# Kernel tuning notes

Hardware: AMD Instinct MI355X
Metric: run time of the kernel (lower is better)

Reference implementation:

```python
import jax, jax.numpy as jnp
import numpy as np

B, C, H, W = 32, 256, 64, 64
LN_EPS = 1e-5

def _conv1x1(x, w, b=None):
    # x: (b,c,h,w), w: (out,c) -> (b,out,h,w)
    y = jnp.einsum('bchw,oc->bohw', x, w)
    if b is not None:
        y = y + b[None, :, None, None]
    return y

def _hsigmoid(t):
    # mmcv HSigmoid: clamp((x + 3) / 6, 0, 1)
    return jnp.clip((t + 3.0) / 6.0, 0.0, 1.0)

def setup_inputs() -> dict:
    key = jax.random.key(0)
    ks = jax.random.split(key, 12)
    s = 0.05
    return {
        'x': jax.random.normal(ks[0], (B, C, H, W), jnp.float32),
        'conv0_w': jax.random.normal(ks[1], (C // 2, C), jnp.float32) * s,
        'conv0_b': jnp.zeros((C // 2,), jnp.float32),
        'bn1_w': jax.random.normal(ks[2], (C, C // 2), jnp.float32) * s,
        'bn1_b': jnp.zeros((C,), jnp.float32),
        'conv1_w': jax.random.normal(ks[3], (1, C), jnp.float32) * s,
        'conv1_b': jnp.zeros((1,), jnp.float32),
        'ln_g': jnp.ones((C,), jnp.float32),
        'ln_b': jnp.zeros((C,), jnp.float32),
        'sk_w1': jax.random.normal(ks[4], (C // 2, C), jnp.float32) * s,
        'sk_w2': jax.random.normal(ks[5], (C, C // 2), jnp.float32) * s,
        'res_w': jax.random.normal(ks[6], (C, C), jnp.float32) * s,
        'res_b': jnp.zeros((C,), jnp.float32),
    }

def reference(x, conv0_w, conv0_b, bn1_w, bn1_b, conv1_w, conv1_b,
              ln_g, ln_b, sk_w1, sk_w2, res_w, res_b):
    b, c, h, w = x.shape
    # ---- channel attention ----
    ca = _conv1x1(x, conv0_w, conv0_b)               # (b, c/2, h, w)
    ca = ca.mean(axis=(2, 3), keepdims=True)          # GAP -> (b, c/2, 1, 1)
    ca = _conv1x1(ca, bn1_w, bn1_b)                   # (b, c, 1, 1)
    ca = _hsigmoid(ca)
    v = ca.reshape(b, c)                              # nchw_to_nlc -> (b, 1, c); LN over c
    mu = v.mean(axis=-1, keepdims=True)
    var = ((v - mu) ** 2).mean(axis=-1, keepdims=True)
    v = (v - mu) * jax.lax.rsqrt(var + LN_EPS) * ln_g + ln_b
    ca = v.reshape(b, c, 1, 1)
    # ---- spatial attention ----
    sa = _conv1x1(x, conv1_w, conv1_b)                # (b, 1, h, w)
    # ---- parallel attention ----
    par = _hsigmoid(sa + ca)                          # (b, c, h, w)
    # ---- sequence attention: bmm outer product (b,c,1)x(b,1,hw) ----
    seq = _hsigmoid(ca * sa)                          # (b, c, h, w)
    # ---- SK module ----
    u = (seq + par).mean(axis=(2, 3), keepdims=True)  # GAP -> (b, c, 1, 1)
    u = _conv1x1(u, sk_w1)                            # (b, c/2, 1, 1), no bias
    u = _conv1x1(u, sk_w2)                            # (b, c, 1, 1), no bias
    a = jax.nn.softmax(u, axis=1)
    sk = seq * a + par * (1.0 - a)
    # softmax over spatial (nchw_to_nlc + Softmax(dim=1))
    sk = jax.nn.softmax(sk.reshape(b, c, h * w), axis=2).reshape(b, c, h, w)
    selected = x * sk
    # ---- self attention ----
    self_attn = selected.sum(axis=(2, 3)).reshape(b, c, 1, 1) + _conv1x1(x, res_w, res_b)
    return selected + self_attn
```

## Files before the change

kernel.cpp:

```cpp
#include <hip/hip_runtime.h>
#include <math.h>

#define B_  32
#define C_  256
#define HW_ 4096
#define LN_EPS 1e-5f

typedef __attribute__((ext_vector_type(4))) float f32x4;
typedef __attribute__((ext_vector_type(8))) short bf16x8;
typedef __attribute__((ext_vector_type(4))) unsigned u32x4;

__device__ __forceinline__ float hsig(float v) {
    return fminf(fmaxf((v + 3.0f) * (1.0f / 6.0f), 0.0f), 1.0f);
}
__device__ __forceinline__ float tval(float ca, float a, float sav) {
    return a * hsig(ca * sav) + (1.0f - a) * hsig(ca + sav);
}
__device__ __forceinline__ unsigned short f2bf(float f) {
    unsigned u = __float_as_uint(f);
    unsigned r = (u + 0x7fffu + ((u >> 16) & 1u)) >> 16;
    return (unsigned short)r;
}
__device__ __forceinline__ float bf2f(unsigned short h) {
    return __uint_as_float(((unsigned)h) << 16);
}


__global__ __launch_bounds__(256) void k_pass1t(
    const float* __restrict__ x, const float* __restrict__ w1,
    float* __restrict__ sa, float* __restrict__ xs_part,
    unsigned short* __restrict__ xbf)
{
    __shared__ float sw1[C_];
    __shared__ float xacc[32 * 257];
    int b = blockIdx.x, hwc = blockIdx.y;
    int tid = threadIdx.x;
    int lane = tid & 63;
    int grp = tid >> 3;
    int hw = hwc * 256 + tid;
    sw1[tid] = w1[tid];
    __syncthreads();
    const float* xb = x + (size_t)b * (C_ * HW_) + hw;
    char* xrow = (char*)xbf + ((size_t)b * HW_ + hw) * 512;
    float sacc = 0.f;
    for (int cb = 0; cb < 4; ++cb) {
        unsigned dwbuf[32];
        #pragma unroll
        for (int cg = 0; cg < 8; ++cg) {
            int c = cb * 64 + cg * 8;
            float v[8];
            #pragma unroll
            for (int j = 0; j < 8; ++j) v[j] = xb[(size_t)(c + j) * HW_];
            float rr[8];
            #pragma unroll
            for (int j = 0; j < 8; ++j) {
                sacc += sw1[c + j] * v[j];
                float r = v[j];
                r += __shfl_xor(r, 1); r += __shfl_xor(r, 2); r += __shfl_xor(r, 4);
                rr[j] = r;
            }
            if ((lane & 7) == 0) {
                #pragma unroll
                for (int j = 0; j < 8; ++j) xacc[grp * 257 + c + j] = rr[j];
            }
            #pragma unroll
            for (int j2 = 0; j2 < 4; ++j2)
                dwbuf[cg * 4 + j2] = (unsigned)f2bf(v[2 * j2]) |
                                     ((unsigned)f2bf(v[2 * j2 + 1]) << 16);
        }
        #pragma unroll
        for (int q = 0; q < 8; ++q) {
            u32x4 t = { dwbuf[q*4+0], dwbuf[q*4+1], dwbuf[q*4+2], dwbuf[q*4+3] };
            *(u32x4*)(xrow + cb * 128 + q * 16) = t;
        }
    }
    sa[(size_t)b * HW_ + hw] = sacc;
    __syncthreads();
    float s = 0.f;
    #pragma unroll
    for (int g = 0; g < 32; ++g) s += xacc[g * 257 + tid];
    xs_part[((size_t)hwc * B_ + b) * C_ + tid] = s;
}

__global__ void k_ca(const float* __restrict__ xs_part, const float* __restrict__ w0,
                     const float* __restrict__ b0, const float* __restrict__ w1,
                     const float* __restrict__ b1, const float* __restrict__ g,
                     const float* __restrict__ be, float* __restrict__ ca,
                     const float* __restrict__ rw, unsigned short* __restrict__ wbs,
                     int nparts) {
    int b = blockIdx.x, tid = threadIdx.x;
    __shared__ float xm[C_], t0[128], red[4];
    float xs = 0.f;
    for (int i = 0; i < nparts; ++i)
        xs += xs_part[((size_t)i * B_ + b) * C_ + tid];
    xm[tid] = xs * (1.0f / HW_);
    __syncthreads();
    if (tid < 128) {
        float s = b0[tid];
        const float* wr = w0 + tid * C_;
        for (int c = 0; c < C_; ++c) s += wr[c] * xm[c];
        t0[tid] = s;
    }
    __syncthreads();
    float s = b1[tid];
    const float* wr = w1 + tid * 128;
    for (int o = 0; o < 128; ++o) s += wr[o] * t0[o];
    float v = hsig(s);
    float sum = v;
    #pragma unroll
    for (int o = 32; o; o >>= 1) sum += __shfl_xor(sum, o);
    if ((tid & 63) == 0) red[tid >> 6] = sum;
    __syncthreads();
    float mu = (red[0] + red[1] + red[2] + red[3]) * (1.0f / C_);
    __syncthreads();
    float d = v - mu;
    float sq = d * d;
    #pragma unroll
    for (int o = 32; o; o >>= 1) sq += __shfl_xor(sq, o);
    if ((tid & 63) == 0) red[tid >> 6] = sq;
    __syncthreads();
    float var = (red[0] + red[1] + red[2] + red[3]) * (1.0f / C_);
    ca[b * C_ + tid] = d * (1.0f / sqrtf(var + LN_EPS)) * g[tid] + be[tid];

    int gid = b * 256 + tid;
    int lane = gid & 63;
    int mi = (gid >> 6) & 3;
    int ks = (gid >> 8) & 7;
    int wv2 = gid >> 11;
    int m = wv2 * 64 + mi * 16 + (lane & 15);
    int kb = ks * 32 + (lane >> 4) * 8;
    const float* src = rw + m * C_ + kb;
    f32x4 a4 = *(const f32x4*)src;
    f32x4 b4 = *(const f32x4*)(src + 4);
    ushort4 o0 = { f2bf(a4.x), f2bf(a4.y), f2bf(a4.z), f2bf(a4.w) };
    ushort4 o1 = { f2bf(b4.x), f2bf(b4.y), f2bf(b4.z), f2bf(b4.w) };
    unsigned short* dst = wbs + (size_t)gid * 8;
    *(ushort4*)dst = o0;
    *(ushort4*)(dst + 4) = o1;
}

__global__ void k_u(const float* __restrict__ sa, const float* __restrict__ ca,
                    const float* __restrict__ b1, float* __restrict__ u) {
    int bc = blockIdx.x;
    int b = bc >> 8;
    int tid = threadIdx.x;
    float cav = ca[bc];
    float bias = b1[0];
    const float* sp = sa + (size_t)b * HW_;
    float s = 0.f;
    for (int i = 0; i < 16; ++i) {
        f32x4 v = *(const f32x4*)(sp + i * 256 + tid * 4);
        #pragma unroll
        for (int j = 0; j < 4; ++j) {
            float sv = v[j] + bias;
            s += hsig(cav * sv) + hsig(cav + sv);
        }
    }
    #pragma unroll
    for (int o = 32; o; o >>= 1) s += __shfl_xor(s, o);
    if (tid == 0) u[bc] = s * (1.0f / HW_);
}

__global__ void k_a(const float* __restrict__ u, const float* __restrict__ w1,
                    const float* __restrict__ w2, float* __restrict__ aout) {
    int b = blockIdx.x, tid = threadIdx.x;
    __shared__ float uu[C_], v0[128], red[4];
    uu[tid] = u[b * C_ + tid];
    __syncthreads();
    if (tid < 128) {
        float s = 0.f;
        const float* wr = w1 + tid * C_;
        for (int c = 0; c < C_; ++c) s += wr[c] * uu[c];
        v0[tid] = s;
    }
    __syncthreads();
    float s = 0.f;
    const float* wr = w2 + tid * 128;
    for (int o = 0; o < 128; ++o) s += wr[o] * v0[o];
    float m = s;
    #pragma unroll
    for (int o = 32; o; o >>= 1) m = fmaxf(m, __shfl_xor(m, o));
    if ((tid & 63) == 0) red[tid >> 6] = m;
    __syncthreads();
    m = fmaxf(fmaxf(red[0], red[1]), fmaxf(red[2], red[3]));
    __syncthreads();
    float e = __expf(s - m);
    float se = e;
    #pragma unroll
    for (int o = 32; o; o >>= 1) se += __shfl_xor(se, o);
    if ((tid & 63) == 0) red[tid >> 6] = se;
    __syncthreads();
    float tot = red[0] + red[1] + red[2] + red[3];
    aout[b * C_ + tid] = e / tot;
}

__global__ __launch_bounds__(512) void k_stats2(
    const unsigned* __restrict__ xbf, const float* __restrict__ sa,
    const float* __restrict__ b1, const float* __restrict__ ca,
    const float* __restrict__ aw, const float* __restrict__ res_b,
    f32x4* __restrict__ st4)
{
    __shared__ float ssa[HW_];
    __shared__ float red[4 * 512];
    int b = blockIdx.x, kpg = blockIdx.y;
    int tid = threadIdx.x;
    int kp_l = tid & 15, hwg = tid >> 4;
    int kp = kpg * 16 + kp_l;
    float bias = b1[0];
    const float* sap = sa + (size_t)b * HW_;
    #pragma unroll
    for (int i = 0; i < 2; ++i) {
        f32x4 v = *(const f32x4*)(sap + i * 2048 + tid * 4);
        v.x += bias; v.y += bias; v.z += bias; v.w += bias;
        *(f32x4*)(ssa + i * 2048 + tid * 4) = v;
    }
    int c0 = b * C_ + 2 * kp;
    float ca0 = ca[c0], ca1 = ca[c0 + 1];
    float a0 = aw[c0],  a1 = aw[c0 + 1];
    __syncthreads();
    const unsigned* xp = xbf + (size_t)b * (HW_ * 128) + kp;
    float se0 = 0.f, xe0 = 0.f, se1 = 0.f, xe1 = 0.f;
    #pragma unroll 4
    for (int r = 0; r < 128; ++r) {
        int hw = r * 32 + hwg;
        unsigned v = xp[(size_t)hw * 128];
        float sav = ssa[hw];
        float e0 = __expf(tval(ca0, a0, sav));
        float e1 = __expf(tval(ca1, a1, sav));
        se0 += e0; se1 += e1;
        xe0 += bf2f((unsigned short)(v & 0xffffu)) * e0;
        xe1 += bf2f((unsigned short)(v >> 16)) * e1;
    }
    red[0 * 512 + hwg * 16 + kp_l] = se0;
    red[1 * 512 + hwg * 16 + kp_l] = se1;
    red[2 * 512 + hwg * 16 + kp_l] = xe0;
    red[3 * 512 + hwg * 16 + kp_l] = xe1;
    __syncthreads();
    if (tid < 32) {
        int kpl = tid & 15, hi = tid >> 4;
        float se = 0.f, xe = 0.f;
        #pragma unroll
        for (int g = 0; g < 32; ++g) {
            se += red[hi * 512 + g * 16 + kpl];
            xe += red[(2 + hi) * 512 + g * 16 + kpl];
        }
        int c = kpg * 32 + 2 * kpl + hi;
        int bc = b * C_ + c;
        float rcp = 1.0f / se;
        f32x4 st = { ca[bc], aw[bc], rcp, xe * rcp + res_b[c] };
        st4[bc] = st;
    }
}

__global__ __launch_bounds__(256, 3) void k_out2(
    const unsigned short* __restrict__ xbf, const unsigned short* __restrict__ wbs,
    const float* __restrict__ sa, const float* __restrict__ b1,
    const f32x4* __restrict__ st4, float* __restrict__ out)
{
    __shared__ __align__(16) unsigned short Bs[64 * 256];
    __shared__ f32x4 sst[C_];
    __shared__ float ssa[64];

    int b = blockIdx.x, tile = blockIdx.y;
    int n0 = tile * 64;
    int tid = threadIdx.x;
    int w = tid >> 6, lane = tid & 63;

    const char* src = (const char*)xbf + (((size_t)(b * 64 + tile)) << 15);
    #pragma unroll
    for (int p = 0; p < 8; ++p) {
        int lbase = p * 4096 + w * 1024;
        int off = lbase + lane * 16;
        int soff = off ^ (((off >> 9) & 7) << 4);
        __builtin_amdgcn_global_load_lds((const unsigned int*)(src + soff),
                                         (unsigned int*)((char*)Bs + lbase), 16, 0, 0);
    }

    bf16x8 af[2][4];
    const bf16x8* wp = (const bf16x8*)wbs;
    #pragma unroll
    for (int ks2 = 0; ks2 < 2; ++ks2)
        #pragma unroll
        for (int mi = 0; mi < 4; ++mi)
            af[ks2][mi] = wp[(size_t)(((w * 8 + ks2) * 4 + mi) * 64 + lane)];

    sst[tid] = st4[b * C_ + tid];
    if (tid < 64) ssa[tid] = sa[(size_t)b * HW_ + n0 + tid] + b1[0];

    __syncthreads();

    f32x4 acc[4][4];
    #pragma unroll
    for (int i = 0; i < 4; ++i)
        #pragma unroll
        for (int j = 0; j < 4; ++j) acc[i][j] = (f32x4){0.f, 0.f, 0.f, 0.f};

    #pragma unroll
    for (int ksg = 0; ksg < 4; ++ksg) {
        #pragma unroll
        for (int ks2 = 0; ks2 < 2; ++ks2) {
            int ks = ksg * 2 + ks2;
            bf16x8 bfr[4];
            #pragma unroll
            for (int ni = 0; ni < 4; ++ni) {
                int n = ni * 16 + (lane & 15);
                int bo = (n * 512 + ks * 64 + (lane >> 4) * 16) ^ ((n & 7) << 4);
                bfr[ni] = *(const bf16x8*)((const char*)Bs + bo);
            }
            #pragma unroll
            for (int mi = 0; mi < 4; ++mi)
                #pragma unroll
                for (int ni = 0; ni < 4; ++ni)
                    acc[mi][ni] = __builtin_amdgcn_mfma_f32_16x16x32_bf16(
                        af[ks2][mi], bfr[ni], acc[mi][ni], 0, 0, 0);
            if (ksg < 3) {
                #pragma unroll
                for (int mi = 0; mi < 4; ++mi)
                    af[ks2][mi] = wp[(size_t)(((w * 8 + (ksg + 1) * 2 + ks2) * 4 + mi) * 64 + lane)];
            }
        }
    }

    float* ob = out + (size_t)b * (C_ * HW_) + n0;
    #pragma unroll
    for (int mi = 0; mi < 4; ++mi) {
        int m0 = w * 64 + mi * 16 + (lane >> 4) * 4;
        f32x4 s0 = sst[m0 + 0];
        f32x4 s1 = sst[m0 + 1];
        f32x4 s2 = sst[m0 + 2];
        f32x4 s3 = sst[m0 + 3];
        #pragma unroll
        for (int ni = 0; ni < 4; ++ni) {
            int n = ni * 16 + (lane & 15);
            float sav = ssa[n];
            int bo = (n * 512 + m0 * 2) ^ ((n & 7) << 4);
            ushort4 xv = *(const ushort4*)((const char*)Bs + bo);
            float o0 = acc[mi][ni][0] + bf2f(xv.x) * (__expf(tval(s0.x, s0.y, sav)) * s0.z) + s0.w;
            float o1 = acc[mi][ni][1] + bf2f(xv.y) * (__expf(tval(s1.x, s1.y, sav)) * s1.z) + s1.w;
            float o2 = acc[mi][ni][2] + bf2f(xv.z) * (__expf(tval(s2.x, s2.y, sav)) * s2.z) + s2.w;
            float o3 = acc[mi][ni][3] + bf2f(xv.w) * (__expf(tval(s3.x, s3.y, sav)) * s3.z) + s3.w;
            ob[(size_t)(m0 + 0) * HW_ + n] = o0;
            ob[(size_t)(m0 + 1) * HW_ + n] = o1;
            ob[(size_t)(m0 + 2) * HW_ + n] = o2;
            ob[(size_t)(m0 + 3) * HW_ + n] = o3;
        }
    }
}


__global__ void k_pass1(const float* __restrict__ x, const float* __restrict__ w1,
                        float* __restrict__ sa, float* __restrict__ xs_part)
{
    int tid = threadIdx.x, wave = tid >> 6, lane = tid & 63;
    int hwq = blockIdx.x, b = blockIdx.y, ct = blockIdx.z;
    int c0 = ct * 32;
    int hw0 = hwq * 1024;
    const float* xb = x + (size_t)b * (C_ * HW_) + hw0 + tid * 4;
    __shared__ float part[32 * 4];
    f32x4 sacc = {0.f, 0.f, 0.f, 0.f};
    #pragma unroll 4
    for (int cc = 0; cc < 32; ++cc) {
        int c = c0 + cc;
        f32x4 v = *(const f32x4*)(xb + (size_t)c * HW_);
        float wv = w1[c];
        sacc += wv * v;
        float h = (v.x + v.y) + (v.z + v.w);
        h += __shfl_xor(h, 32); h += __shfl_xor(h, 16); h += __shfl_xor(h, 8);
        h += __shfl_xor(h, 4);  h += __shfl_xor(h, 2);  h += __shfl_xor(h, 1);
        if (lane == 0) part[cc * 4 + wave] = h;
    }
    float* sp = sa + (size_t)b * HW_ + hw0 + tid * 4;
    atomicAdd(sp + 0, sacc.x);
    atomicAdd(sp + 1, sacc.y);
    atomicAdd(sp + 2, sacc.z);
    atomicAdd(sp + 3, sacc.w);
    __syncthreads();
    if (tid < 32)
        xs_part[((size_t)hwq * B_ + b) * C_ + c0 + tid] =
            part[tid * 4 + 0] + part[tid * 4 + 1] + part[tid * 4 + 2] + part[tid * 4 + 3];
}

__global__ void k_stats(const float* __restrict__ x, const float* __restrict__ sa,
                        const float* __restrict__ b1,
                        const float* __restrict__ ca, const float* __restrict__ aw,
                        const float* __restrict__ res_b, f32x4* __restrict__ st4) {
    int bc = blockIdx.x;
    int b = bc >> 8, c = bc & 255;
    int tid = threadIdx.x;
    float cav = ca[bc], av = aw[bc];
    float bias = b1[0];
    const float* sp = sa + (size_t)b * HW_;
    const float* xp = x + (size_t)bc * HW_;
    float se = 0.f, xe = 0.f;
    #pragma unroll
    for (int i = 0; i < 4; ++i) {
        f32x4 s4 = *(const f32x4*)(sp + i * 1024 + tid * 4);
        f32x4 x4 = *(const f32x4*)(xp + i * 1024 + tid * 4);
        #pragma unroll
        for (int j = 0; j < 4; ++j) {
            float e = __expf(tval(cav, av, s4[j] + bias));
            se += e;
            xe += x4[j] * e;
        }
    }
    __shared__ float red[4], red2[4];
    #pragma unroll
    for (int o = 32; o; o >>= 1) { se += __shfl_xor(se, o); xe += __shfl_xor(xe, o); }
    if ((tid & 63) == 0) { red[tid >> 6] = se; red2[tid >> 6] = xe; }
    __syncthreads();
    if (tid == 0) {
        float S = red[0] + red[1] + red[2] + red[3];
        float X = red2[0] + red2[1] + red2[2] + red2[3];
        float rcp = 1.0f / S;
        f32x4 st = { cav, av, rcp, X * rcp + res_b[c] };
        st4[bc] = st;
    }
}

__global__ __launch_bounds__(256, 2) void k_out(
    const float* __restrict__ x, const unsigned short* __restrict__ wbs,
    const float* __restrict__ sa, const float* __restrict__ b1,
    const f32x4* __restrict__ st4, float* __restrict__ out)
{
    __shared__ __align__(16) unsigned short Bs[64 * 256];
    __shared__ f32x4 sst[C_];
    __shared__ float ssa[64];

    int b = blockIdx.x, tile = blockIdx.y;
    int n0 = tile * 64;
    int tid = threadIdx.x;
    int w = tid >> 6, lane = tid & 63;

    const float* xb = x + (size_t)b * (C_ * HW_);

    bf16x8 af[8][4];
    #pragma unroll
    for (int ks = 0; ks < 8; ++ks)
        #pragma unroll
        for (int mi = 0; mi < 4; ++mi)
            af[ks][mi] = *(const bf16x8*)(wbs + (size_t)(((w * 8 + ks) * 4 + mi) * 64 + lane) * 8);

    sst[tid] = st4[b * C_ + tid];
    if (tid < 64) ssa[tid] = sa[(size_t)b * HW_ + n0 + tid] + b1[0];

    #pragma unroll
    for (int p2 = 0; p2 < 8; ++p2) {
        int id = p2 * 256 + tid;
        int kp = id >> 4;
        int tcn = id & 15;
        const float* g0 = xb + (size_t)(2 * kp) * HW_ + n0 + 4 * tcn;
        f32x4 v0 = *(const f32x4*)g0;
        f32x4 v1 = *(const f32x4*)(g0 + HW_);
        #pragma unroll
        for (int i = 0; i < 4; ++i) {
            int n = 4 * tcn + i;
            unsigned val = (unsigned)f2bf(v0[i]) | ((unsigned)f2bf(v1[i]) << 16);
            int bo = (n * 512 + kp * 4) ^ ((n & 7) << 4);
            *(unsigned*)((char*)Bs + bo) = val;
        }
    }
    __syncthreads();

    f32x4 acc[4][4];
    #pragma unroll
    for (int i = 0; i < 4; ++i)
        #pragma unroll
        for (int j = 0; j < 4; ++j) acc[i][j] = (f32x4){0.f, 0.f, 0.f, 0.f};

    #pragma unroll
    for (int ks = 0; ks < 8; ++ks) {
        bf16x8 bfr[4];
        #pragma unroll
        for (int ni = 0; ni < 4; ++ni) {
            int n = ni * 16 + (lane & 15);
            int bo = (n * 512 + ks * 64 + (lane >> 4) * 16) ^ ((n & 7) << 4);
            bfr[ni] = *(const bf16x8*)((const char*)Bs + bo);
        }
        #pragma unroll
        for (int mi = 0; mi < 4; ++mi)
            #pragma unroll
            for (int ni = 0; ni < 4; ++ni)
                acc[mi][ni] = __builtin_amdgcn_mfma_f32_16x16x32_bf16(
                    af[ks][mi], bfr[ni], acc[mi][ni], 0, 0, 0);
    }

    float* ob = out + (size_t)b * (C_ * HW_) + n0;
    #pragma unroll
    for (int mi = 0; mi < 4; ++mi) {
        int m0 = w * 64 + mi * 16 + (lane >> 4) * 4;
        f32x4 s0 = sst[m0 + 0];
        f32x4 s1 = sst[m0 + 1];
        f32x4 s2 = sst[m0 + 2];
        f32x4 s3 = sst[m0 + 3];
        #pragma unroll
        for (int ni = 0; ni < 4; ++ni) {
            int n = ni * 16 + (lane & 15);
            float sav = ssa[n];
            int bo = (n * 512 + m0 * 2) ^ ((n & 7) << 4);
            ushort4 xv = *(const ushort4*)((const char*)Bs + bo);
            float o0 = acc[mi][ni][0] + bf2f(xv.x) * (__expf(tval(s0.x, s0.y, sav)) * s0.z) + s0.w;
            float o1 = acc[mi][ni][1] + bf2f(xv.y) * (__expf(tval(s1.x, s1.y, sav)) * s1.z) + s1.w;
            float o2 = acc[mi][ni][2] + bf2f(xv.z) * (__expf(tval(s2.x, s2.y, sav)) * s2.z) + s2.w;
            float o3 = acc[mi][ni][3] + bf2f(xv.w) * (__expf(tval(s3.x, s3.y, sav)) * s3.z) + s3.w;
            ob[(size_t)(m0 + 0) * HW_ + n] = o0;
            ob[(size_t)(m0 + 1) * HW_ + n] = o1;
            ob[(size_t)(m0 + 2) * HW_ + n] = o2;
            ob[(size_t)(m0 + 3) * HW_ + n] = o3;
        }
    }
}

extern "C" void kernel_launch(void* const* d_in, const int* in_sizes, int n_in,
                              void* d_out, int out_size, void* d_ws, size_t ws_size,
                              hipStream_t stream) {
    (void)in_sizes; (void)n_in; (void)out_size;
    const float* x   = (const float*)d_in[0];
    const float* c0w = (const float*)d_in[1];
    const float* c0b = (const float*)d_in[2];
    const float* b1w = (const float*)d_in[3];
    const float* b1b = (const float*)d_in[4];
    const float* c1w = (const float*)d_in[5];
    const float* c1b = (const float*)d_in[6];
    const float* lng = (const float*)d_in[7];
    const float* lnb = (const float*)d_in[8];
    const float* sw1 = (const float*)d_in[9];
    const float* sw2 = (const float*)d_in[10];
    const float* rw  = (const float*)d_in[11];
    const float* rb  = (const float*)d_in[12];
    float* out = (float*)d_out;
    float* ws = (float*)d_ws;

    const size_t NEW_WS_FLOATS = (size_t)352256 + 16777216;
    if (ws_size >= NEW_WS_FLOATS * sizeof(float)) {
        float* sa      = ws;
        float* xs_part = ws + 131072;
        float* ca      = ws + 262144;
        float* u       = ws + 270336;
        float* aw      = ws + 278528;
        f32x4* st4     = (f32x4*)(ws + 286720);
        unsigned short* wbs = (unsigned short*)(ws + 319488);
        unsigned short* xbf = (unsigned short*)(ws + 352256);

        hipLaunchKernelGGL(k_pass1t, dim3(32, 16), dim3(256), 0, stream, x, c1w, sa, xs_part, xbf);
        hipLaunchKernelGGL(k_ca,     dim3(32),     dim3(256), 0, stream, xs_part, c0w, c0b, b1w, b1b, lng, lnb, ca, rw, wbs, 16);
        hipLaunchKernelGGL(k_u,      dim3(8192),   dim3(64),  0, stream, sa, ca, c1b, u);
        hipLaunchKernelGGL(k_a,      dim3(32),     dim3(256), 0, stream, u, sw1, sw2, aw);
        hipLaunchKernelGGL(k_stats2, dim3(32, 8),  dim3(512), 0, stream, (const unsigned*)xbf, sa, c1b, ca, aw, rb, st4);
        hipLaunchKernelGGL(k_out2,   dim3(32, 64), dim3(256), 0, stream, xbf, wbs, sa, c1b, st4, out);
    } else {
        float* sa      = ws;
        float* xs_part = ws + 131072;
        float* ca      = ws + 163840;
        float* u       = ws + 172032;
        float* aw      = ws + 180224;
        f32x4* st4     = (f32x4*)(ws + 188416);
        unsigned short* wbs = (unsigned short*)(ws + 221184);

        hipMemsetAsync(sa, 0, (size_t)B_ * HW_ * sizeof(float), stream);
        hipLaunchKernelGGL(k_pass1, dim3(4, 32, 8), dim3(256), 0, stream, x, c1w, sa, xs_part);
        hipLaunchKernelGGL(k_ca,    dim3(32),       dim3(256), 0, stream, xs_part, c0w, c0b, b1w, b1b, lng, lnb, ca, rw, wbs, 4);
        hipLaunchKernelGGL(k_u,     dim3(8192),     dim3(64),  0, stream, sa, ca, c1b, u);
        hipLaunchKernelGGL(k_a,     dim3(32),       dim3(256), 0, stream, u, sw1, sw2, aw);
        hipLaunchKernelGGL(k_stats, dim3(8192),     dim3(256), 0, stream, x, sa, c1b, ca, aw, rb, st4);
        hipLaunchKernelGGL(k_out,   dim3(32, 64),   dim3(256), 0, stream, x, wbs, sa, c1b, st4, out);
    }
}
```

Before: 179.8 us.

## Store bf16 copy of x in channel-major layout and transpose inside output kernel

The bf16 copy of x is now written in the original NCHW order with coalesced vector stores, instead of the transposed HW-major layout that needed per-thread 512-byte rows. The stats kernel becomes one block per (batch, channel) reading contiguous rows. The output kernel now loads channel rows into registers and transposes them into the swizzled LDS tile itself, replacing the async global-to-LDS copy, and uses a new XOR swizzle. This trades cheaper pass1 writes and stats reads for extra register pressure and LDS transpose work in the GEMM kernel.

```diff
diff --git a/kernel.cpp b/kernel.cpp
--- a/kernel.cpp
+++ b/kernel.cpp
@@ -9,6 +9,7 @@
 typedef __attribute__((ext_vector_type(4))) float f32x4;
 typedef __attribute__((ext_vector_type(8))) short bf16x8;
 typedef __attribute__((ext_vector_type(4))) unsigned u32x4;
+typedef __attribute__((ext_vector_type(2))) unsigned u32x2;
 
 __device__ __forceinline__ float hsig(float v) {
     return fminf(fmaxf((v + 3.0f) * (1.0f / 6.0f), 0.0f), 1.0f);
@@ -24,62 +25,44 @@
 __device__ __forceinline__ float bf2f(unsigned short h) {
     return __uint_as_float(((unsigned)h) << 16);
 }
-
-
-__global__ __launch_bounds__(256) void k_pass1t(
+__device__ __forceinline__ int bswz(int n) {
+    return ((n & 7) ^ ((n >> 3) & 7)) << 4;
+}
+
+
+__global__ __launch_bounds__(256) void k_pass1b(
     const float* __restrict__ x, const float* __restrict__ w1,
     float* __restrict__ sa, float* __restrict__ xs_part,
     unsigned short* __restrict__ xbf)
 {
     __shared__ float sw1[C_];
-    __shared__ float xacc[32 * 257];
-    int b = blockIdx.x, hwc = blockIdx.y;
-    int tid = threadIdx.x;
-    int lane = tid & 63;
-    int grp = tid >> 3;
-    int hw = hwc * 256 + tid;
+    __shared__ float sred[4][256];
+    __shared__ float xsl[C_];
+    int hwq = blockIdx.x, b = blockIdx.y;
+    int tid = threadIdx.x, w = tid >> 6, l = tid & 63;
+    int hw0 = hwq * 256;
     sw1[tid] = w1[tid];
     __syncthreads();
-    const float* xb = x + (size_t)b * (C_ * HW_) + hw;
-    char* xrow = (char*)xbf + ((size_t)b * HW_ + hw) * 512;
-    float sacc = 0.f;
-    for (int cb = 0; cb < 4; ++cb) {
-        unsigned dwbuf[32];
-        #pragma unroll
-        for (int cg = 0; cg < 8; ++cg) {
-            int c = cb * 64 + cg * 8;
-            float v[8];
-            #pragma unroll
-            for (int j = 0; j < 8; ++j) v[j] = xb[(size_t)(c + j) * HW_];
-            float rr[8];
-            #pragma unroll
-            for (int j = 0; j < 8; ++j) {
-                sacc += sw1[c + j] * v[j];
-                float r = v[j];
-                r += __shfl_xor(r, 1); r += __shfl_xor(r, 2); r += __shfl_xor(r, 4);
-                rr[j] = r;
-            }
-            if ((lane & 7) == 0) {
-                #pragma unroll
-                for (int j = 0; j < 8; ++j) xacc[grp * 257 + c + j] = rr[j];
-            }
-            #pragma unroll
-            for (int j2 = 0; j2 < 4; ++j2)
-                dwbuf[cg * 4 + j2] = (unsigned)f2bf(v[2 * j2]) |
-                                     ((unsigned)f2bf(v[2 * j2 + 1]) << 16);
-        }
-        #pragma unroll
-        for (int q = 0; q < 8; ++q) {
-            u32x4 t = { dwbuf[q*4+0], dwbuf[q*4+1], dwbuf[q*4+2], dwbuf[q*4+3] };
-            *(u32x4*)(xrow + cb * 128 + q * 16) = t;
-        }
-    }
-    sa[(size_t)b * HW_ + hw] = sacc;
-    __syncthreads();
-    float s = 0.f;
-    #pragma unroll
-    for (int g = 0; g < 32; ++g) s += xacc[g * 257 + tid];
-    xs_part[((size_t)hwc * B_ + b) * C_ + tid] = s;
+    const float* xb = x + (size_t)b * (C_ * HW_) + hw0 + l * 4;
+    unsigned short* xo = xbf + (size_t)b * (C_ * HW_) + hw0 + l * 4;
+    f32x4 sacc = {0.f, 0.f, 0.f, 0.f};
+    #pragma unroll 4
+    for (int i = 0; i < 64; ++i) {
+        int c = i * 4 + w;
+        f32x4 v = *(const f32x4*)(xb + (size_t)c * HW_);
+        sacc += sw1[c] * v;
+        ushort4 o = { f2bf(v.x), f2bf(v.y), f2bf(v.z), f2bf(v.w) };
+        *(ushort4*)(xo + (size_t)c * HW_) = o;
+        float h = (v.x + v.y) + (v.z + v.w);
+        h += __shfl_xor(h, 32); h += __shfl_xor(h, 16); h += __shfl_xor(h, 8);
+        h += __shfl_xor(h, 4);  h += __shfl_xor(h, 2);  h += __shfl_xor(h, 1);
+        if (l == 0) xsl[c] = h;
+    }
+    *(f32x4*)&sred[w][l * 4] = sacc;
+    __syncthreads();
+    sa[(size_t)b * HW_ + hw0 + tid] =
+        sred[0][tid] + sred[1][tid] + sred[2][tid] + sred[3][tid];
+    xs_part[((size_t)hwq * B_ + b) * C_ + tid] = xsl[tid];
 }
 
 __global__ void k_ca(const float* __restrict__ xs_part, const float* __restrict__ w0,
@@ -194,65 +177,49 @@
     aout[b * C_ + tid] = e / tot;
 }
 
-__global__ __launch_bounds__(512) void k_stats2(
-    const unsigned* __restrict__ xbf, const float* __restrict__ sa,
-    const float* __restrict__ b1, const float* __restrict__ ca,
-    const float* __restrict__ aw, const float* __restrict__ res_b,
-    f32x4* __restrict__ st4)
-{
-    __shared__ float ssa[HW_];
-    __shared__ float red[4 * 512];
-    int b = blockIdx.x, kpg = blockIdx.y;
+__global__ void k_stats3(const unsigned short* __restrict__ xbf, const float* __restrict__ sa,
+                         const float* __restrict__ b1,
+                         const float* __restrict__ ca, const float* __restrict__ aw,
+                         const float* __restrict__ res_b, f32x4* __restrict__ st4) {
+    int bc = blockIdx.x;
+    int b = bc >> 8, c = bc & 255;
     int tid = threadIdx.x;
-    int kp_l = tid & 15, hwg = tid >> 4;
-    int kp = kpg * 16 + kp_l;
+    float cav = ca[bc], av = aw[bc];
     float bias = b1[0];
-    const float* sap = sa + (size_t)b * HW_;
-    #pragma unroll
-    for (int i = 0; i < 2; ++i) {
-        f32x4 v = *(const f32x4*)(sap + i * 2048 + tid * 4);
-        v.x += bias; v.y += bias; v.z += bias; v.w += bias;
-        *(f32x4*)(ssa + i * 2048 + tid * 4) = v;
-    }
-    int c0 = b * C_ + 2 * kp;
-    float ca0 = ca[c0], ca1 = ca[c0 + 1];
-    float a0 = aw[c0],  a1 = aw[c0 + 1];
-    __syncthreads();
-    const unsigned* xp = xbf + (size_t)b * (HW_ * 128) + kp;
-    float se0 = 0.f, xe0 = 0.f, se1 = 0.f, xe1 = 0.f;
-    #pragma unroll 4
-    for (int r = 0; r < 128; ++r) {
-        int hw = r * 32 + hwg;
-        unsigned v = xp[(size_t)hw * 128];
-        float sav = ssa[hw];
-        float e0 = __expf(tval(ca0, a0, sav));
-        float e1 = __expf(tval(ca1, a1, sav));
-        se0 += e0; se1 += e1;
-        xe0 += bf2f((unsigned short)(v & 0xffffu)) * e0;
-        xe1 += bf2f((unsigned short)(v >> 16)) * e1;
-    }
-    red[0 * 512 + hwg * 16 + kp_l] = se0;
-    red[1 * 512 + hwg * 16 + kp_l] = se1;
-    red[2 * 512 + hwg * 16 + kp_l] = xe0;
-    red[3 * 512 + hwg * 16 + kp_l] = xe1;
-    __syncthreads();
-    if (tid < 32) {
-        int kpl = tid & 15, hi = tid >> 4;
-        float se = 0.f, xe = 0.f;
-        #pragma unroll
-        for (int g = 0; g < 32; ++g) {
-            se += red[hi * 512 + g * 16 + kpl];
-            xe += red[(2 + hi) * 512 + g * 16 + kpl];
-        }
-        int c = kpg * 32 + 2 * kpl + hi;
-        int bc = b * C_ + c;
-        float rcp = 1.0f / se;
-        f32x4 st = { ca[bc], aw[bc], rcp, xe * rcp + res_b[c] };
+    const float* sp = sa + (size_t)b * HW_;
+    const unsigned* xp = (const unsigned*)(xbf + (size_t)bc * HW_);
+    float se = 0.f, xe = 0.f;
+    #pragma unroll
+    for (int i = 0; i < 4; ++i) {
+        f32x4 s4 = *(const f32x4*)(sp + i * 1024 + tid * 4);
+        u32x2 x2 = *(const u32x2*)(xp + i * 512 + tid * 2);
+        float xv[4];
+        xv[0] = bf2f((unsigned short)(x2[0] & 0xffffu));
+        xv[1] = bf2f((unsigned short)(x2[0] >> 16));
+        xv[2] = bf2f((unsigned short)(x2[1] & 0xffffu));
+        xv[3] = bf2f((unsigned short)(x2[1] >> 16));
+        #pragma unroll
+        for (int j = 0; j < 4; ++j) {
+            float e = __expf(tval(cav, av, s4[j] + bias));
+            se += e;
+            xe += xv[j] * e;
+        }
+    }
+    __shared__ float red[4], red2[4];
+    #pragma unroll
+    for (int o = 32; o; o >>= 1) { se += __shfl_xor(se, o); xe += __shfl_xor(xe, o); }
+    if ((tid & 63) == 0) { red[tid >> 6] = se; red2[tid >> 6] = xe; }
+    __syncthreads();
+    if (tid == 0) {
+        float S = red[0] + red[1] + red[2] + red[3];
+        float X = red2[0] + red2[1] + red2[2] + red2[3];
+        float rcp = 1.0f / S;
+        f32x4 st = { cav, av, rcp, X * rcp + res_b[c] };
         st4[bc] = st;
     }
 }
 
-__global__ __launch_bounds__(256, 3) void k_out2(
+__global__ __launch_bounds__(256, 3) void k_out3(
     const unsigned short* __restrict__ xbf, const unsigned short* __restrict__ wbs,
     const float* __restrict__ sa, const float* __restrict__ b1,
     const f32x4* __restrict__ st4, float* __restrict__ out)
@@ -265,15 +232,17 @@
     int n0 = tile * 64;
     int tid = threadIdx.x;
     int w = tid >> 6, lane = tid & 63;
-
-    const char* src = (const char*)xbf + (((size_t)(b * 64 + tile)) << 15);
-    #pragma unroll
-    for (int p = 0; p < 8; ++p) {
-        int lbase = p * 4096 + w * 1024;
-        int off = lbase + lane * 16;
-        int soff = off ^ (((off >> 9) & 7) << 4);
-        __builtin_amdgcn_global_load_lds((const unsigned int*)(src + soff),
-                                         (unsigned int*)((char*)Bs + lbase), 16, 0, 0);
+    int hwc = tid & 7;
+    int cq  = tid >> 3;
+
+    const unsigned short* xb = xbf + (size_t)b * (C_ * HW_) + n0 + hwc * 8;
+    u32x4 ld[2][4];
+    #pragma unroll
+    for (int it = 0; it < 2; ++it) {
+        int c0 = it * 128 + cq * 4;
+        #pragma unroll
+        for (int r = 0; r < 4; ++r)
+            ld[it][r] = *(const u32x4*)(xb + (size_t)(c0 + r) * HW_);
     }
 
     bf16x8 af[2][4];
@@ -287,6 +256,27 @@
     sst[tid] = st4[b * C_ + tid];
     if (tid < 64) ssa[tid] = sa[(size_t)b * HW_ + n0 + tid] + b1[0];
 
+    #pragma unroll
+    for (int it = 0; it < 2; ++it) {
+        int kp0 = it * 64 + cq * 2;
+        #pragma unroll
+        for (int e = 0; e < 8; ++e) {
+            int n = hwc * 8 + e;
+            unsigned a0 = ld[it][0][e >> 1], b0v = ld[it][1][e >> 1];
+            unsigned a1 = ld[it][2][e >> 1], b1v = ld[it][3][e >> 1];
+            unsigned d0, d1;
+            if (e & 1) {
+                d0 = (a0 >> 16) | (b0v & 0xffff0000u);
+                d1 = (a1 >> 16) | (b1v & 0xffff0000u);
+            } else {
+                d0 = (a0 & 0xffffu) | (b0v << 16);
+                d1 = (a1 & 0xffffu) | (b1v << 16);
+            }
+            int bo = (n * 512 + kp0 * 4) ^ bswz(n);
+            u32x2 dd = { d0, d1 };
+            *(u32x2*)((char*)Bs + bo) = dd;
+        }
+    }
     __syncthreads();
 
     f32x4 acc[4][4];
@@ -304,7 +294,7 @@
             #pragma unroll
             for (int ni = 0; ni < 4; ++ni) {
                 int n = ni * 16 + (lane & 15);
-                int bo = (n * 512 + ks * 64 + (lane >> 4) * 16) ^ ((n & 7) << 4);
+                int bo = (n * 512 + ks * 64 + (lane >> 4) * 16) ^ bswz(n);
                 bfr[ni] = *(const bf16x8*)((const char*)Bs + bo);
             }
             #pragma unroll
@@ -333,7 +323,7 @@
         for (int ni = 0; ni < 4; ++ni) {
             int n = ni * 16 + (lane & 15);
             float sav = ssa[n];
-            int bo = (n * 512 + m0 * 2) ^ ((n & 7) << 4);
+            int bo = (n * 512 + m0 * 2) ^ bswz(n);
             ushort4 xv = *(const ushort4*)((const char*)Bs + bo);
             float o0 = acc[mi][ni][0] + bf2f(xv.x) * (__expf(tval(s0.x, s0.y, sav)) * s0.z) + s0.w;
             float o1 = acc[mi][ni][1] + bf2f(xv.y) * (__expf(tval(s1.x, s1.y, sav)) * s1.z) + s1.w;
@@ -541,12 +531,12 @@
         unsigned short* wbs = (unsigned short*)(ws + 319488);
         unsigned short* xbf = (unsigned short*)(ws + 352256);
 
-        hipLaunchKernelGGL(k_pass1t, dim3(32, 16), dim3(256), 0, stream, x, c1w, sa, xs_part, xbf);
+        hipLaunchKernelGGL(k_pass1b, dim3(16, 32), dim3(256), 0, stream, x, c1w, sa, xs_part, xbf);
         hipLaunchKernelGGL(k_ca,     dim3(32),     dim3(256), 0, stream, xs_part, c0w, c0b, b1w, b1b, lng, lnb, ca, rw, wbs, 16);
         hipLaunchKernelGGL(k_u,      dim3(8192),   dim3(64),  0, stream, sa, ca, c1b, u);
         hipLaunchKernelGGL(k_a,      dim3(32),     dim3(256), 0, stream, u, sw1, sw2, aw);
-        hipLaunchKernelGGL(k_stats2, dim3(32, 8),  dim3(512), 0, stream, (const unsigned*)xbf, sa, c1b, ca, aw, rb, st4);
-        hipLaunchKernelGGL(k_out2,   dim3(32, 64), dim3(256), 0, stream, xbf, wbs, sa, c1b, st4, out);
+        hipLaunchKernelGGL(k_stats3, dim3(8192),   dim3(256), 0, stream, xbf, sa, c1b, ca, aw, rb, st4);
+        hipLaunchKernelGGL(k_out3,   dim3(32, 64), dim3(256), 0, stream, xbf, wbs, sa, c1b, st4, out);
     } else {
         float* sa      = ws;
         float* xs_part = ws + 131072;
```

Result: faster. 170.2 us (-5.3%).
